# Kernel tuning notes

Hardware: AMD Instinct MI355X
Metric: run time of the kernel (lower is better)

## Reference

```python
import jax, jax.numpy as jnp
import numpy as np

D_MODEL = 1024
N_HEADS = 16
D_H = D_MODEL // N_HEADS
B, T = 4, 2048
NEG_INF = jnp.finfo(jnp.float32).min


def setup_inputs() -> dict:
    key = jax.random.key(0)
    ks = jax.random.split(key, 9)
    s = 1.0 / np.sqrt(D_MODEL)
    inp = {
        "x": jax.random.normal(ks[0], (B, T, D_MODEL), dtype=jnp.float32),
        "pad_mask": jnp.zeros((B, T), dtype=bool),
        "Wq": jax.random.uniform(ks[1], (D_MODEL, D_MODEL), jnp.float32, -s, s),
        "bq": jax.random.uniform(ks[2], (D_MODEL,), jnp.float32, -s, s),
        "Wk": jax.random.uniform(ks[3], (D_MODEL, D_MODEL), jnp.float32, -s, s),
        "bk": jax.random.uniform(ks[4], (D_MODEL,), jnp.float32, -s, s),
        "Wv": jax.random.uniform(ks[5], (D_MODEL, D_MODEL), jnp.float32, -s, s),
        "bv": jax.random.uniform(ks[6], (D_MODEL,), jnp.float32, -s, s),
        "Wo": jax.random.uniform(ks[7], (D_MODEL, D_MODEL), jnp.float32, -s, s),
        "bo": jax.random.uniform(ks[8], (D_MODEL,), jnp.float32, -s, s),
    }
    return inp


def reference(x, pad_mask, Wq, bq, Wk, bk, Wv, bv, Wo, bo):
    b, t, _ = x.shape
    # torch Linear: y = x @ W.T + b
    def proj(W, bias):
        y = jnp.einsum("btd,ed->bte", x, W) + bias
        return y.reshape(b, t, N_HEADS, D_H).transpose(0, 2, 1, 3)  # (B,H,T,d_h)

    Q, K, V = proj(Wq, bq), proj(Wk, bk), proj(Wv, bv)
    S = jnp.einsum("bhqd,bhkd->bhqk", Q, K) / jnp.sqrt(jnp.float32(D_H))
    causal = jnp.triu(jnp.ones((t, t), dtype=bool), k=1)[None, None]
    S = jnp.where(causal, NEG_INF, S)
    S = jnp.where(pad_mask[:, None, None, :], NEG_INF, S)
    A = jax.nn.softmax(S, axis=-1)
    Y = jnp.einsum("bhqk,bhkd->bhqd", A, V)
    Y = Y.transpose(0, 2, 1, 3).reshape(b, t, D_MODEL)
    O = jnp.einsum("btd,ed->bte", Y, Wo) + bo
    return O
```

## Files before the change

kernel.cpp:

```cpp
#include <hip/hip_runtime.h>
#include <stdint.h>
#include <stddef.h>

#define Tq 2048
#define DM 1024

typedef unsigned short u16;
typedef __bf16 bf16x8 __attribute__((ext_vector_type(8)));
typedef float f32x4 __attribute__((ext_vector_type(4)));
typedef unsigned short u16x8 __attribute__((ext_vector_type(8)));
typedef unsigned short u16x4 __attribute__((ext_vector_type(4)));

__device__ __forceinline__ float bf2f(u16 h) {
    union { unsigned int u; float f; } c; c.u = ((unsigned int)h) << 16; return c.f;
}
__device__ __forceinline__ u16 f2bf(float f) {
    union { float f; unsigned int u; } c; c.f = f;
    unsigned int u = c.u;
    return (u16)((u + 0x7fffu + ((u >> 16) & 1u)) >> 16);
}

__device__ __forceinline__ float exp2_native(float x) {
    float r; asm("v_exp_f32 %0, %1" : "=v"(r) : "v"(x)); return r;
}

#define GLD(gp, lp) __builtin_amdgcn_global_load_lds(                                  \
        (const __attribute__((address_space(1))) void*)(gp),                           \
        (__attribute__((address_space(3))) void*)(lp), 16, 0, 0)

__device__ __forceinline__ int sniff_fp32(const u16* xs) {
    const int lane = threadIdx.x & 63;
    const u16 u = xs[lane];
    const int e = (u >> 7) & 0xFF;
    unsigned long long m = __ballot(e >= 160);
    return __popcll(m) >= 4;
}

__device__ __forceinline__ void cvt_body(const void* src, u16* dst, int i0, int fmt) {
    if (fmt) {
        const float* s = (const float*)src;
        float4 a = *(const float4*)(s + i0);
        float4 b = *(const float4*)(s + i0 + 4);
        u16x8 o;
        o[0] = f2bf(a.x); o[1] = f2bf(a.y); o[2] = f2bf(a.z); o[3] = f2bf(a.w);
        o[4] = f2bf(b.x); o[5] = f2bf(b.y); o[6] = f2bf(b.z); o[7] = f2bf(b.w);
        *(u16x8*)(dst + i0) = o;
    } else {
        *(u16x8*)(dst + i0) = *(const u16x8*)((const u16*)src + i0);
    }
}

__global__ void cvt_all(const void* __restrict__ x,
                        const void* s0, const void* s1, const void* s2, const void* s3,
                        const void* t0, const void* t1, const void* t2, const void* t3,
                        u16* __restrict__ xc, u16* __restrict__ dstW, float* __restrict__ dstB,
                        const u16* __restrict__ xs, int* flag) {
    const int fmt = sniff_fp32(xs);
    int bx = blockIdx.x;
    if (bx < 4096) {
        if (bx == 0 && threadIdx.x == 0) *flag = fmt;
        const int i0 = (bx * 256 + threadIdx.x) * 8;
        cvt_body(x, xc, i0, fmt);
    } else {
        bx -= 4096;
        const int wsel = bx >> 9;
        const int bi   = bx & 511;
        const void* s = (wsel == 0) ? s0 : (wsel == 1) ? s1 : (wsel == 2) ? s2 : s3;
        u16* d = dstW + (size_t)wsel * (DM * DM);
        const int i0 = (bi * 256 + threadIdx.x) * 8;
        cvt_body(s, d, i0, fmt);
        if (bi == 0) {
            const void* bs = (wsel == 0) ? t0 : (wsel == 1) ? t1 : (wsel == 2) ? t2 : t3;
            float* db = dstB + (size_t)wsel * DM;
            const int j0 = threadIdx.x * 4;
            if (fmt) {
                *(float4*)(db + j0) = *(const float4*)((const float*)bs + j0);
            } else {
                const u16* ss = (const u16*)bs;
                db[j0+0] = bf2f(ss[j0+0]); db[j0+1] = bf2f(ss[j0+1]);
                db[j0+2] = bf2f(ss[j0+2]); db[j0+3] = bf2f(ss[j0+3]);
            }
        }
    }
}

#define NT 16

__global__ __launch_bounds__(512, 1) void gemm256(
    const u16* __restrict__ A,
    const u16* __restrict__ W0, const u16* __restrict__ W1, const u16* __restrict__ W2,
    const float* __restrict__ b0, const float* __restrict__ b1, const float* __restrict__ b2,
    u16* o0, u16* o1, u16* o2,
    const int* __restrict__ flag, int mode)
{
    __shared__ u16 LB[3][24576];

    const int K = DM;
    const int j = blockIdx.y;
    const int which = (mode == 0) ? (j >> 2) : 0;
    const u16* Wp     = (which == 0) ? W0 : (which == 1) ? W1 : W2;
    const float* bias = (which == 0) ? b0 : (which == 1) ? b1 : b2;
    u16* out          = (which == 0) ? o0 : (which == 1) ? o1 : o2;
    const int jn = (mode == 0) ? (j & 3) : j;
    const int m0 = blockIdx.x * 128, n0 = jn * 256;

    const int tid  = threadIdx.x;
    const int w    = tid >> 6, lane = tid & 63;
    const int wm   = w >> 2, wn = w & 3;
    const int l4   = lane & 15, quad = lane >> 4;
    const int rsub = lane >> 3;
    const int colE = ((lane & 7) ^ rsub) << 3;

#define STAGE_A(kt, bf) do {                                                            \
        const int k0s = (kt) * 64;                                                      \
        _Pragma("unroll")                                                               \
        for (int c = 0; c < 2; ++c) {                                                   \
            const int row = c * 64 + w * 8 + rsub;                                      \
            GLD(A + (size_t)(m0 + row) * K + k0s + colE,                                \
                (char*)&LB[bf][0] + c * 8192 + w * 1024);                               \
        }                                                                               \
        {   const int row = w * 8 + rsub;                                               \
            GLD(Wp + (size_t)(n0 + row) * K + k0s + colE,                               \
                (char*)&LB[bf][0] + 16384 + w * 1024); }                                \
    } while (0)
#define STAGE_B(kt, bf) do {                                                            \
        const int k0s = (kt) * 64;                                                      \
        _Pragma("unroll")                                                               \
        for (int c = 1; c < 4; ++c) {                                                   \
            const int row = c * 64 + w * 8 + rsub;                                      \
            GLD(Wp + (size_t)(n0 + row) * K + k0s + colE,                               \
                (char*)&LB[bf][0] + 16384 + c * 8192 + w * 1024);                       \
        }                                                                               \
    } while (0)

    f32x4 acc[4][4] = {};

    STAGE_A(0, 0); STAGE_B(0, 0);
    STAGE_A(1, 1); STAGE_B(1, 1);
    __syncthreads();

    for (int t = 0; t < NT; ++t) {
        const int cur = t % 3;
        const int nxt = (t + 2) % 3;
        const u16* Ab = &LB[cur][0];
        const u16* Bb = &LB[cur][8192];
        const int swz = (l4 & 7) << 3;
        const bool pf = (t + 2 < NT);

        if (pf) STAGE_A(t + 2, nxt);
        {
            bf16x8 af[4], bfr[4];
            const int kq = (quad * 8) ^ swz;
#pragma unroll
            for (int m = 0; m < 4; ++m)
                af[m] = *(const bf16x8*)&Ab[(wm * 64 + m * 16 + l4) * 64 + kq];
#pragma unroll
            for (int n = 0; n < 4; ++n)
                bfr[n] = *(const bf16x8*)&Bb[(wn * 64 + n * 16 + l4) * 64 + kq];
            __builtin_amdgcn_s_setprio(1);
#pragma unroll
            for (int m = 0; m < 4; ++m)
#pragma unroll
                for (int n = 0; n < 4; ++n)
                    acc[m][n] = __builtin_amdgcn_mfma_f32_16x16x32_bf16(af[m], bfr[n], acc[m][n], 0, 0, 0);
            __builtin_amdgcn_s_setprio(0);
        }

        if (pf) STAGE_B(t + 2, nxt);
        {
            bf16x8 af[4], bfr[4];
            const int kq = (32 + quad * 8) ^ swz;
#pragma unroll
            for (int m = 0; m < 4; ++m)
                af[m] = *(const bf16x8*)&Ab[(wm * 64 + m * 16 + l4) * 64 + kq];
#pragma unroll
            for (int n = 0; n < 4; ++n)
                bfr[n] = *(const bf16x8*)&Bb[(wn * 64 + n * 16 + l4) * 64 + kq];
            __builtin_amdgcn_s_setprio(1);
#pragma unroll
            for (int m = 0; m < 4; ++m)
#pragma unroll
                for (int n = 0; n < 4; ++n)
                    acc[m][n] = __builtin_amdgcn_mfma_f32_16x16x32_bf16(af[m], bfr[n], acc[m][n], 0, 0, 0);
            __builtin_amdgcn_s_setprio(0);
        }

        if (t + 1 < NT) __syncthreads();
    }
#undef STAGE_A
#undef STAGE_B

    const int ofmt = (mode == 1) ? *flag : 0;
    const float SCQ = 0.18033688011112042f;

#pragma unroll
    for (int n = 0; n < 4; ++n) {
        const int colw = n0 + wn * 64 + n * 16 + l4;
        const float bv = bias[colw];
#pragma unroll
        for (int m = 0; m < 4; ++m) {
            const int mb = m0 + wm * 64 + m * 16 + quad * 4;
            if (mode == 0) {
                const int bb = mb >> 11, t0 = mb & 2047;
                const int h = colw >> 6, d = colw & 63;
                if (which == 2) {
                    u16x4 pk;
#pragma unroll
                    for (int reg = 0; reg < 4; ++reg) pk[reg] = f2bf(acc[m][n][reg] + bv);
                    *(u16x4*)&out[((size_t)(bb * 16 + h) * 64 + d) * 2048 + t0] = pk;
                } else {
                    const float s = (which == 0) ? SCQ : 1.0f;
#pragma unroll
                    for (int reg = 0; reg < 4; ++reg)
                        out[(size_t)((bb * 16 + h) * 2048 + (t0 + reg)) * 64 + d] =
                            f2bf((acc[m][n][reg] + bv) * s);
                }
            } else if (ofmt) {
#pragma unroll
                for (int reg = 0; reg < 4; ++reg)
                    ((float*)out)[(size_t)(mb + reg) * DM + colw] = acc[m][n][reg] + bv;
            } else {
#pragma unroll
                for (int reg = 0; reg < 4; ++reg)
                    out[(size_t)(mb + reg) * DM + colw] = f2bf(acc[m][n][reg] + bv);
            }
        }
    }
}

#define LSTR 72

__global__ __launch_bounds__(256, 2) void attn4(
    const u16* __restrict__ Qb, const u16* __restrict__ Kb, const u16* __restrict__ VT,
    const unsigned char* __restrict__ pad,
    u16* __restrict__ Y)
{
    __shared__ u16 Klds[2][64 * LSTR];
    __shared__ u16 Vtl [2][64 * LSTR];
    __shared__ u16 Pl  [4][64 * LSTR];
    __shared__ unsigned char padl[2][64];

    const int nb = blockIdx.y;
    const int bh = blockIdx.x;
    const int b = bh >> 4, h = bh & 15;
    const u16* Qp  = Qb + (size_t)bh * (Tq * 64);
    const u16* Kp  = Kb + (size_t)bh * (Tq * 64);
    const u16* VTp = VT + (size_t)bh * (64 * Tq);

    const int tid = threadIdx.x;
    const int w = tid >> 6, lane = tid & 63;
    const int l4 = lane & 15, quad = lane >> 4;

    const int qt[4] = { nb, nb + 8, 23 - nb, 31 - nb };

    bf16x8 qf[4][2];
#pragma unroll
    for (int g = 0; g < 4; ++g) {
        const u16* r = Qp + (size_t)(qt[g] * 64 + w * 16 + l4) * 64 + quad * 8;
        qf[g][0] = *(const bf16x8*)r;
        qf[g][1] = *(const bf16x8*)(r + 32);
    }

    bf16x8 ones;
#pragma unroll
    for (int e = 0; e < 8; ++e) ones[e] = (__bf16)1.0f;

    f32x4 o[4][4] = {};
    f32x4 ls[4] = {};

    const int srow = tid >> 2;
    const int sc   = (tid & 3) * 16;

    u16x8 kr0, kr1, vr0, vr1; unsigned char pr = 0;
    {
        const u16* kg = Kp + (size_t)srow * 64 + sc;
        kr0 = *(const u16x8*)kg; kr1 = *(const u16x8*)(kg + 8);
        const u16* vg = VTp + (size_t)srow * Tq + sc;
        vr0 = *(const u16x8*)vg; vr1 = *(const u16x8*)(vg + 8);
        if (tid < 64) pr = pad[(size_t)b * Tq + tid];
    }
    *(u16x8*)&Klds[0][srow * LSTR + sc]     = kr0;
    *(u16x8*)&Klds[0][srow * LSTR + sc + 8] = kr1;
    *(u16x8*)&Vtl [0][srow * LSTR + sc]     = vr0;
    *(u16x8*)&Vtl [0][srow * LSTR + sc + 8] = vr1;
    if (tid < 64) padl[0][tid] = pr;

    const int ktmax = qt[3];

    for (int kt = 0; kt <= ktmax; ++kt) {
        const int cur = kt & 1;
        const int k0 = kt * 64;
        __syncthreads();
        if (kt < ktmax) {
            const u16* kg = Kp + (size_t)(k0 + 64 + srow) * 64 + sc;
            kr0 = *(const u16x8*)kg; kr1 = *(const u16x8*)(kg + 8);
            const u16* vg = VTp + (size_t)srow * Tq + k0 + 64 + sc;
            vr0 = *(const u16x8*)vg; vr1 = *(const u16x8*)(vg + 8);
            if (tid < 64) pr = pad[(size_t)b * Tq + k0 + 64 + tid];
        }

        const bool anypad = __any((int)(padl[cur][lane] != 0));

        bf16x8 kf[2][4];
#pragma unroll
        for (int c = 0; c < 2; ++c)
#pragma unroll
            for (int n = 0; n < 4; ++n)
                kf[c][n] = *(const bf16x8*)&Klds[cur][(n * 16 + l4) * LSTR + c * 32 + quad * 8];

#pragma unroll
        for (int g = 0; g < 4; ++g) {
            if (kt > qt[g]) continue;
            f32x4 sacc[4] = {};
            __builtin_amdgcn_s_setprio(1);
#pragma unroll
            for (int c = 0; c < 2; ++c)
#pragma unroll
                for (int n = 0; n < 4; ++n)
                    sacc[n] = __builtin_amdgcn_mfma_f32_16x16x32_bf16(qf[g][c], kf[c][n], sacc[n], 0, 0, 0);
            __builtin_amdgcn_s_setprio(0);
            u16* Pg = &Pl[g][0];
            if (kt == qt[g] || anypad) {
                bool pm[4];
#pragma unroll
                for (int n = 0; n < 4; ++n) pm[n] = (padl[cur][n * 16 + l4] != 0);
                const int qr = qt[g] * 64 + w * 16 + quad * 4;
#pragma unroll
                for (int r = 0; r < 4; ++r) {
#pragma unroll
                    for (int n = 0; n < 4; ++n) {
                        const int kgi = k0 + n * 16 + l4;
                        const bool msk = (kgi > qr + r) || pm[n];
                        const float p = msk ? 0.0f : exp2_native(sacc[n][r]);
                        *(__bf16*)&Pg[(w * 16 + quad * 4 + r) * LSTR + n * 16 + l4] = (__bf16)p;
                    }
                }
            } else {
#pragma unroll
                for (int r = 0; r < 4; ++r) {
#pragma unroll
                    for (int n = 0; n < 4; ++n) {
                        const float p = exp2_native(sacc[n][r]);
                        *(__bf16*)&Pg[(w * 16 + quad * 4 + r) * LSTR + n * 16 + l4] = (__bf16)p;
                    }
                }
            }
        }

        bf16x8 vf[2][4];
#pragma unroll
        for (int c = 0; c < 2; ++c)
#pragma unroll
            for (int t = 0; t < 4; ++t)
                vf[c][t] = *(const bf16x8*)&Vtl[cur][(t * 16 + l4) * LSTR + c * 32 + quad * 8];

#pragma unroll
        for (int g = 0; g < 4; ++g) {
            if (kt > qt[g]) continue;
            __builtin_amdgcn_s_setprio(1);
#pragma unroll
            for (int c = 0; c < 2; ++c) {
                bf16x8 pf = *(const bf16x8*)&Pl[g][(w * 16 + l4) * LSTR + c * 32 + quad * 8];
#pragma unroll
                for (int t = 0; t < 4; ++t)
                    o[g][t] = __builtin_amdgcn_mfma_f32_16x16x32_bf16(pf, vf[c][t], o[g][t], 0, 0, 0);
                ls[g] = __builtin_amdgcn_mfma_f32_16x16x32_bf16(pf, ones, ls[g], 0, 0, 0);
            }
            __builtin_amdgcn_s_setprio(0);
        }

        if (kt < ktmax) {
            *(u16x8*)&Klds[cur ^ 1][srow * LSTR + sc]     = kr0;
            *(u16x8*)&Klds[cur ^ 1][srow * LSTR + sc + 8] = kr1;
            *(u16x8*)&Vtl [cur ^ 1][srow * LSTR + sc]     = vr0;
            *(u16x8*)&Vtl [cur ^ 1][srow * LSTR + sc + 8] = vr1;
            if (tid < 64) padl[cur ^ 1][tid] = pr;
        }
    }

#pragma unroll
    for (int g = 0; g < 4; ++g)
#pragma unroll
        for (int r = 0; r < 4; ++r) {
            const float inv = 1.0f / ls[g][r];
            u16* y = Y + (size_t)(b * Tq + (qt[g] * 64 + w * 16 + quad * 4 + r)) * DM + h * 64;
#pragma unroll
            for (int t = 0; t < 4; ++t)
                *(__bf16*)&y[t * 16 + l4] = (__bf16)(o[g][t][r] * inv);
        }
}

extern "C" void kernel_launch(void* const* d_in, const int* in_sizes, int n_in,
                              void* d_out, int out_size, void* d_ws, size_t ws_size,
                              hipStream_t stream) {
    const void* x  = d_in[0];
    const unsigned char* pad = (const unsigned char*)d_in[1];
    const void* Wq = d_in[2];
    const void* bq = d_in[3];
    const void* Wk = d_in[4];
    const void* bk = d_in[5];
    const void* Wv = d_in[6];
    const void* bv = d_in[7];
    const void* Wo = d_in[8];
    const void* bo = d_in[9];
    const u16* xs = (const u16*)x;

    const size_t NEL = (size_t)8192 * 1024;
    const size_t WEL = (size_t)1024 * 1024;

    int* flag   = (int*)d_ws;
    u16* base16 = (u16*)((char*)d_ws + 256);
    u16* xc     = base16;
    u16* Wc     = base16 + NEL;
    float* bf_  = (float*)(base16 + NEL + 4*WEL);
    u16* Qb     = (u16*)(bf_ + 4096);
    u16* Kb     = Qb + NEL;
    u16* VT     = Kb + NEL;
    u16* Yb     = xc;

    cvt_all<<<dim3(6144), 256, 0, stream>>>(x, Wq, Wk, Wv, Wo, bq, bk, bv, bo,
                                            xc, Wc, bf_, xs, flag);

    gemm256<<<dim3(64, 12), 512, 0, stream>>>(xc, Wc, Wc + WEL, Wc + 2*WEL,
                                              bf_, bf_ + 1024, bf_ + 2048,
                                              Qb, Kb, VT, flag, 0);
    attn4<<<dim3(64, 8), 256, 0, stream>>>(Qb, Kb, VT, pad, Yb);
    gemm256<<<dim3(64, 4), 512, 0, stream>>>(Yb, Wc + 3*WEL, Wc + 3*WEL, Wc + 3*WEL,
                                             bf_ + 3072, bf_ + 3072, bf_ + 3072,
                                             (u16*)d_out, nullptr, nullptr, flag, 1);
}
```

Measured before the change: 248.4 us.

## Split attention blocks to two query tiles and single-buffer K/V LDS

Each attention block now handles two paired query tiles (nb, 31-nb) instead of four, and the grid doubles to 64x16 blocks, so there is more parallelism and less per-block register state. The K/V/pad LDS tiles go from double-buffered to single-buffered, with a barrier before and after each LDS store. Register prefetch from global memory is kept. The intent is higher occupancy and less LDS use, at the cost of an extra sync per iteration, less overlap between loads and compute, and K/V being reloaded by twice as many blocks.

```diff
diff --git a/kernel.cpp b/kernel.cpp
--- a/kernel.cpp
+++ b/kernel.cpp
@@ -235,10 +235,10 @@
     const unsigned char* __restrict__ pad,
     u16* __restrict__ Y)
 {
-    __shared__ u16 Klds[2][64 * LSTR];
-    __shared__ u16 Vtl [2][64 * LSTR];
-    __shared__ u16 Pl  [4][64 * LSTR];
-    __shared__ unsigned char padl[2][64];
+    __shared__ u16 Klds[64 * LSTR];
+    __shared__ u16 Vtl [64 * LSTR];
+    __shared__ u16 Pl  [2][64 * LSTR];
+    __shared__ unsigned char padl[64];
 
     const int nb = blockIdx.y;
     const int bh = blockIdx.x;
@@ -251,11 +251,11 @@
     const int w = tid >> 6, lane = tid & 63;
     const int l4 = lane & 15, quad = lane >> 4;
 
-    const int qt[4] = { nb, nb + 8, 23 - nb, 31 - nb };
-
-    bf16x8 qf[4][2];
-#pragma unroll
-    for (int g = 0; g < 4; ++g) {
+    const int qt[2] = { nb, 31 - nb };
+
+    bf16x8 qf[2][2];
+#pragma unroll
+    for (int g = 0; g < 2; ++g) {
         const u16* r = Qp + (size_t)(qt[g] * 64 + w * 16 + l4) * 64 + quad * 8;
         qf[g][0] = *(const bf16x8*)r;
         qf[g][1] = *(const bf16x8*)(r + 32);
@@ -265,8 +265,8 @@
 #pragma unroll
     for (int e = 0; e < 8; ++e) ones[e] = (__bf16)1.0f;
 
-    f32x4 o[4][4] = {};
-    f32x4 ls[4] = {};
+    f32x4 o[2][4] = {};
+    f32x4 ls[2] = {};
 
     const int srow = tid >> 2;
     const int sc   = (tid & 3) * 16;
@@ -279,17 +279,17 @@
         vr0 = *(const u16x8*)vg; vr1 = *(const u16x8*)(vg + 8);
         if (tid < 64) pr = pad[(size_t)b * Tq + tid];
     }
-    *(u16x8*)&Klds[0][srow * LSTR + sc]     = kr0;
-    *(u16x8*)&Klds[0][srow * LSTR + sc + 8] = kr1;
-    *(u16x8*)&Vtl [0][srow * LSTR + sc]     = vr0;
-    *(u16x8*)&Vtl [0][srow * LSTR + sc + 8] = vr1;
-    if (tid < 64) padl[0][tid] = pr;
-
-    const int ktmax = qt[3];
+
+    const int ktmax = qt[1];
 
     for (int kt = 0; kt <= ktmax; ++kt) {
-        const int cur = kt & 1;
         const int k0 = kt * 64;
+        __syncthreads();
+        *(u16x8*)&Klds[srow * LSTR + sc]     = kr0;
+        *(u16x8*)&Klds[srow * LSTR + sc + 8] = kr1;
+        *(u16x8*)&Vtl [srow * LSTR + sc]     = vr0;
+        *(u16x8*)&Vtl [srow * LSTR + sc + 8] = vr1;
+        if (tid < 64) padl[tid] = pr;
         __syncthreads();
         if (kt < ktmax) {
             const u16* kg = Kp + (size_t)(k0 + 64 + srow) * 64 + sc;
@@ -299,17 +299,17 @@
             if (tid < 64) pr = pad[(size_t)b * Tq + k0 + 64 + tid];
         }
 
-        const bool anypad = __any((int)(padl[cur][lane] != 0));
+        const bool anypad = __any((int)(padl[lane] != 0));
 
         bf16x8 kf[2][4];
 #pragma unroll
         for (int c = 0; c < 2; ++c)
 #pragma unroll
             for (int n = 0; n < 4; ++n)
-                kf[c][n] = *(const bf16x8*)&Klds[cur][(n * 16 + l4) * LSTR + c * 32 + quad * 8];
-
-#pragma unroll
-        for (int g = 0; g < 4; ++g) {
+                kf[c][n] = *(const bf16x8*)&Klds[(n * 16 + l4) * LSTR + c * 32 + quad * 8];
+
+#pragma unroll
+        for (int g = 0; g < 2; ++g) {
             if (kt > qt[g]) continue;
             f32x4 sacc[4] = {};
             __builtin_amdgcn_s_setprio(1);
@@ -323,7 +323,7 @@
             if (kt == qt[g] || anypad) {
                 bool pm[4];
 #pragma unroll
-                for (int n = 0; n < 4; ++n) pm[n] = (padl[cur][n * 16 + l4] != 0);
+                for (int n = 0; n < 4; ++n) pm[n] = (padl[n * 16 + l4] != 0);
                 const int qr = qt[g] * 64 + w * 16 + quad * 4;
 #pragma unroll
                 for (int r = 0; r < 4; ++r) {
@@ -352,10 +352,10 @@
         for (int c = 0; c < 2; ++c)
 #pragma unroll
             for (int t = 0; t < 4; ++t)
-                vf[c][t] = *(const bf16x8*)&Vtl[cur][(t * 16 + l4) * LSTR + c * 32 + quad * 8];
-
-#pragma unroll
-        for (int g = 0; g < 4; ++g) {
+                vf[c][t] = *(const bf16x8*)&Vtl[(t * 16 + l4) * LSTR + c * 32 + quad * 8];
+
+#pragma unroll
+        for (int g = 0; g < 2; ++g) {
             if (kt > qt[g]) continue;
             __builtin_amdgcn_s_setprio(1);
 #pragma unroll
@@ -368,18 +368,10 @@
             }
             __builtin_amdgcn_s_setprio(0);
         }
-
-        if (kt < ktmax) {
-            *(u16x8*)&Klds[cur ^ 1][srow * LSTR + sc]     = kr0;
-            *(u16x8*)&Klds[cur ^ 1][srow * LSTR + sc + 8] = kr1;
-            *(u16x8*)&Vtl [cur ^ 1][srow * LSTR + sc]     = vr0;
-            *(u16x8*)&Vtl [cur ^ 1][srow * LSTR + sc + 8] = vr1;
-            if (tid < 64) padl[cur ^ 1][tid] = pr;
-        }
-    }
-
-#pragma unroll
-    for (int g = 0; g < 4; ++g)
+    }
+
+#pragma unroll
+    for (int g = 0; g < 2; ++g)
 #pragma unroll
         for (int r = 0; r < 4; ++r) {
             const float inv = 1.0f / ls[g][r];
@@ -424,7 +416,7 @@
     gemm256<<<dim3(64, 12), 512, 0, stream>>>(xc, Wc, Wc + WEL, Wc + 2*WEL,
                                               bf_, bf_ + 1024, bf_ + 2048,
                                               Qb, Kb, VT, flag, 0);
-    attn4<<<dim3(64, 8), 256, 0, stream>>>(Qb, Kb, VT, pad, Yb);
+    attn4<<<dim3(64, 16), 256, 0, stream>>>(Qb, Kb, VT, pad, Yb);
     gemm256<<<dim3(64, 4), 512, 0, stream>>>(Yb, Wc + 3*WEL, Wc + 3*WEL, Wc + 3*WEL,
                                              bf_ + 3072, bf_ + 3072, bf_ + 3072,
                                              (u16*)d_out, nullptr, nullptr, flag, 1);
```

Result: slower. 256.6 us (+3.3%).
